# Performance work log

Measured on AMD Instinct MI355X. Metric: run time of the kernel, lower is better.

## Reference

```python
import jax, jax.numpy as jnp
import numpy as np

FIELD = 7  # field_size


def _conv1x1(x, w):
    # x: [b,c,h,w], w: [c_out,c_in] (1x1 conv, no bias)
    return jnp.einsum('bchw,oc->bohw', x, w)


def _patches(x, f):
    # torch unfold with 'same' padding: output [b, c*f*f, h, w], channel-major
    # (feature index = c*f*f + kh*f + kw), matching KAIR extract_image_patches
    # layout for odd f / stride 1 (symmetric pad (f-1)//2).
    return jax.lax.conv_general_dilated_patches(
        x, filter_shape=(f, f), window_strides=(1, 1), padding='SAME',
        dimension_numbers=('NCHW', 'OIHW', 'NCHW'))


def setup_inputs() -> dict:
    key = jax.random.key(0)
    k0, k1, k2, k3, k4 = jax.random.split(key, 5)
    c, ci = 256, 128
    b, h, w = 4, 64, 64
    s = 1.0 / np.sqrt(c)
    si = 1.0 / np.sqrt(ci)
    return {
        'x': jax.random.normal(k0, (b, c, h, w), dtype=jnp.float32),
        'w_phi': jax.random.normal(k1, (ci, c), dtype=jnp.float32) * s,
        'w_theta': jax.random.normal(k2, (ci, c), dtype=jnp.float32) * s,
        'w_g': jax.random.normal(k3, (ci, c), dtype=jnp.float32) * s,
        'w_mask': jax.random.normal(k4, (c, ci), dtype=jnp.float32) * si,
    }


def reference(x, w_phi, w_theta, w_g, w_mask):
    b, c, h, w = x.shape
    ci = w_phi.shape[0]
    f = FIELD
    kk = f * f

    x_phi = _conv1x1(x, w_phi)      # [b,ci,h,w]
    x_g = _conv1x1(x, w_g)          # [b,ci,h,w]
    x_theta = _conv1x1(x, w_theta)  # [b,ci,h,w]

    # theta: unsqueeze(-2) then permute(0,2,4,3,1) -> [b,h,w,1,ci]
    q = jnp.transpose(x_theta, (0, 2, 3, 1))[:, :, :, None, :]

    # phi patches: [b, ci*kk, h, w] reshaped (row-major, faithful to torch
    # reshape of the unfold output) to [b,h,w,ci,kk]
    p_phi = _patches(x_phi, f).reshape(b, h, w, ci, kk)
    scores = jnp.matmul(q, p_phi)                 # [b,h,w,1,kk]
    attn = jax.nn.softmax(scores, axis=1)         # softmax over dim=1 (h), faithful

    p_g = _patches(x_g, f).reshape(b, h, w, kk, ci)
    out = jnp.matmul(attn, p_g)                   # [b,h,w,1,ci]

    # permute(0,4,3,1,2).view(b,ci,h,w)
    y = jnp.transpose(out, (0, 4, 3, 1, 2)).reshape(b, ci, h, w)
    mask = _conv1x1(y, w_mask)                    # [b,c,h,w]
    return mask + x
```

## Files before the change

### kernel.cpp

```cpp
#include <hip/hip_runtime.h>


#define PLANE    5040
#define A_BATCH  645120

typedef __attribute__((ext_vector_type(8))) short short8;
typedef __attribute__((ext_vector_type(4))) float floatx4;

__device__ __forceinline__ float bf2f(unsigned short u) {
    union { unsigned int i; float f; } v; v.i = ((unsigned int)u) << 16; return v.f;
}
__device__ __forceinline__ unsigned short f2bf(float f) {
    union { float f; unsigned int i; } v; v.f = f;
    unsigned int r = v.i + 0x7FFFu + ((v.i >> 16) & 1u);
    return (unsigned short)(r >> 16);
}

__global__ __launch_bounds__(256) void prep_kernel(
    const float* __restrict__ x,
    const float* __restrict__ w_phi,
    const float* __restrict__ w_theta,
    const float* __restrict__ w_g,
    const float* __restrict__ w_mask,
    unsigned short* __restrict__ xp_hi,
    unsigned short* __restrict__ xp_lo,
    unsigned short* __restrict__ w3p_hi,
    unsigned short* __restrict__ w3p_lo,
    unsigned short* __restrict__ wmp_hi,
    unsigned short* __restrict__ wmp_lo,
    uint4* __restrict__ zero_region)
{
    const int tid = threadIdx.x;
    const int bx = blockIdx.x;

    if (bx < 1024) {
        const int b  = bx >> 8;
        const int kt = (bx >> 6) & 3;
        const int pt = bx & 63;
        __shared__ float tile[64][65];
        #pragma unroll
        for (int i = 0; i < 16; ++i) {
            int lin = tid + i * 256;
            int kk = lin >> 6, pp = lin & 63;
            tile[kk][pp] = x[(b * 256 + kt * 64 + kk) * 4096 + pt * 64 + pp];
        }
        __syncthreads();
        #pragma unroll
        for (int i = 0; i < 16; ++i) {
            int lin = tid + i * 256;
            int frag = lin >> 9;
            int idx  = lin & 511;
            int kbL  = frag >> 2;
            int ptL  = frag & 3;
            int j    = idx & 7;
            int n    = (idx >> 3) & 15;
            int quad = idx >> 7;
            float f = tile[kbL * 32 + quad * 8 + j][ptL * 16 + n];
            unsigned short h = f2bf(f);
            int addr = ((b * 8 + kt * 2 + kbL) * 256 + pt * 4 + ptL) * 512 + idx;
            xp_hi[addr] = h;
            xp_lo[addr] = f2bf(f - bf2f(h));
        }
    } else {
        const int wid = (bx - 1024) * 256 + tid;
        for (int e = wid; e < 98304; e += 32768) {
            int frag = e >> 9;
            int idx  = e & 511;
            int nt16 = frag >> 3, kb = frag & 7;
            int j = idx & 7, m = (idx >> 3) & 15, quad = idx >> 7;
            int n = nt16 * 16 + m;
            int k = kb * 32 + quad * 8 + j;
            float v = (n < 128) ? w_phi[n * 256 + k]
                    : (n < 256) ? w_theta[(n - 128) * 256 + k]
                                : w_g[(n - 256) * 256 + k];
            unsigned short h = f2bf(v);
            w3p_hi[e] = h;
            w3p_lo[e] = f2bf(v - bf2f(h));
        }
        {
            int e = wid;
            int frag = e >> 9;
            int idx  = e & 511;
            int ot16 = frag >> 2, kb = frag & 3;
            int j = idx & 7, m = (idx >> 3) & 15, quad = idx >> 7;
            float v = w_mask[(ot16 * 16 + m) * 128 + kb * 32 + quad * 8 + j];
            unsigned short h = f2bf(v);
            wmp_hi[e] = h;
            wmp_lo[e] = f2bf(v - bf2f(h));
        }
        const uint4 z = make_uint4(0u, 0u, 0u, 0u);
        for (int i = wid; i < 645120; i += 32768) zero_region[i] = z;
    }
}

__global__ __launch_bounds__(256) void conv3_mfma_kernel(
    const unsigned short* __restrict__ xp_hi,
    const unsigned short* __restrict__ xp_lo,
    const unsigned short* __restrict__ w3p_hi,
    const unsigned short* __restrict__ w3p_lo,
    unsigned short* __restrict__ A_phi,
    unsigned short* __restrict__ theta_bf,
    unsigned short* __restrict__ A_g)
{
    const int tid = threadIdx.x;
    const int w   = tid >> 6;
    const int ln  = tid & 63;
    const int lm  = ln & 15;
    const int quad = ln >> 4;
    const int bx = blockIdx.x;
    const int nt = blockIdx.y;
    const int b  = blockIdx.z;
    const int nt16a = nt * 8 + w;
    const int nt16b = nt * 8 + 4 + w;
    const int lnofs = ln * 8;

    floatx4 accA[4] = {{0.f,0.f,0.f,0.f},{0.f,0.f,0.f,0.f},
                       {0.f,0.f,0.f,0.f},{0.f,0.f,0.f,0.f}};
    floatx4 accB[4] = {{0.f,0.f,0.f,0.f},{0.f,0.f,0.f,0.f},
                       {0.f,0.f,0.f,0.f},{0.f,0.f,0.f,0.f}};

    #pragma unroll
    for (int kb = 0; kb < 8; ++kb) {
        const int aoffA = (nt16a * 8 + kb) * 512 + lnofs;
        const int aoffB = (nt16b * 8 + kb) * 512 + lnofs;
        const int boff  = ((b * 8 + kb) * 256 + bx * 4) * 512 + lnofs;
        short8 ahA = *reinterpret_cast<const short8*>(w3p_hi + aoffA);
        short8 alA = *reinterpret_cast<const short8*>(w3p_lo + aoffA);
        short8 ahB = *reinterpret_cast<const short8*>(w3p_hi + aoffB);
        short8 alB = *reinterpret_cast<const short8*>(w3p_lo + aoffB);
        short8 bh[4], bl[4];
        #pragma unroll
        for (int ct = 0; ct < 4; ++ct) {
            bh[ct] = *reinterpret_cast<const short8*>(xp_hi + boff + ct * 512);
            bl[ct] = *reinterpret_cast<const short8*>(xp_lo + boff + ct * 512);
        }
        #pragma unroll
        for (int ct = 0; ct < 4; ++ct) {
            accA[ct] = __builtin_amdgcn_mfma_f32_16x16x32_bf16(ahA, bh[ct], accA[ct], 0, 0, 0);
            accA[ct] = __builtin_amdgcn_mfma_f32_16x16x32_bf16(ahA, bl[ct], accA[ct], 0, 0, 0);
            accA[ct] = __builtin_amdgcn_mfma_f32_16x16x32_bf16(alA, bh[ct], accA[ct], 0, 0, 0);
            accB[ct] = __builtin_amdgcn_mfma_f32_16x16x32_bf16(ahB, bh[ct], accB[ct], 0, 0, 0);
            accB[ct] = __builtin_amdgcn_mfma_f32_16x16x32_bf16(ahB, bl[ct], accB[ct], 0, 0, 0);
            accB[ct] = __builtin_amdgcn_mfma_f32_16x16x32_bf16(alB, bh[ct], accB[ct], 0, 0, 0);
        }
    }

    const int py = bx;
    if (nt == 1) {
        #pragma unroll
        for (int ct = 0; ct < 4; ++ct) {
            const int p = bx * 64 + ct * 16 + lm;
            #pragma unroll
            for (int reg = 0; reg < 4; ++reg) {
                const int r = w * 16 + quad * 4 + reg;
                theta_bf[(b * 4096 + p) * 128 + r]      = f2bf(accA[ct][reg]);
                theta_bf[(b * 4096 + p) * 128 + r + 64] = f2bf(accB[ct][reg]);
            }
        }
    } else {
        unsigned short* __restrict__ A = (nt == 0) ? A_phi : A_g;
        #pragma unroll
        for (int ct = 0; ct < 4; ++ct) {
            const int pxx = ct * 16 + lm;
            #pragma unroll
            for (int reg = 0; reg < 4; ++reg) {
                const int r = w * 16 + quad * 4 + reg;
                A[b * A_BATCH + r * PLANE + (py + 3) * 72 + pxx + 4] =
                    f2bf(accA[ct][reg]);
                A[b * A_BATCH + (r + 64) * PLANE + (py + 3) * 72 + pxx + 4] =
                    f2bf(accB[ct][reg]);
            }
        }
    }
}

__global__ __launch_bounds__(256, 8) void scores_kernel(
    const unsigned short* __restrict__ Apad,
    const unsigned short* __restrict__ theta_bf,
    float* __restrict__ scores)
{
    const int w  = threadIdx.x >> 6;
    const int ln = threadIdx.x & 63;
    const int s  = blockIdx.x * 4 + w;
    const int b  = blockIdx.y;

    __shared__ float th[4][128];
    {
        const unsigned short* tb = theta_bf + (b * 4096 + s) * 128;
        th[w][ln]      = bf2f(tb[ln]);
        th[w][ln + 64] = bf2f(tb[ln + 64]);
    }
    __syncthreads();

    const unsigned short* __restrict__ Ab = Apad + b * A_BATCH;

    const int base  = s * 6272;
    const int ch_lo = base >> 12;
    const unsigned B1 = (unsigned)(ch_lo + 1) << 12;
    const unsigned B2 = (unsigned)(ch_lo + 2) << 12;
    const int d1 = (int)B1 - base;
    const int d2 = d1 + 4096;

    int A1 = d1 / 49;
    int A2 = (d1 + 48) / 49;
    int C1 = d2 / 49;        if (C1 > 128) C1 = 128;
    int C2 = (d2 + 48) / 49; if (C2 > 128) C2 = 128;

    unsigned OFFv[3];
    #pragma unroll
    for (int i = 0; i < 3; ++i) {
        int ch = ch_lo + i;
        int c0 = ch / 49; if (c0 > 127) c0 = 127;
        int rr = ch - c0 * 49;
        int kh = rr / 7;
        int kw = rr - kh * 7;
        OFFv[i] = (unsigned)(c0 * PLANE + kh * 72 + kw + 1);
    }

    unsigned F = (unsigned)(base + ln);
    float acc = 0.f;

    {
        const unsigned OFF_ = OFFv[0];
        #pragma unroll 4
        for (int cc = 0; cc < A1; ++cc) {
            unsigned p = F & 4095u;
            unsigned a = OFF_ + p + ((p >> 6) << 3);
            acc = fmaf(th[w][cc], bf2f(Ab[a]), acc);
            F += 49u;
        }
    }
    for (int cc = A1; cc < A2; ++cc) {
        unsigned OFF_ = (F >= B1) ? OFFv[1] : OFFv[0];
        unsigned p = F & 4095u;
        unsigned a = OFF_ + p + ((p >> 6) << 3);
        acc = fmaf(th[w][cc], bf2f(Ab[a]), acc);
        F += 49u;
    }
    {
        const unsigned OFF_ = OFFv[1];
        #pragma unroll 4
        for (int cc = A2; cc < C1; ++cc) {
            unsigned p = F & 4095u;
            unsigned a = OFF_ + p + ((p >> 6) << 3);
            acc = fmaf(th[w][cc], bf2f(Ab[a]), acc);
            F += 49u;
        }
    }
    for (int cc = C1; cc < C2; ++cc) {
        unsigned OFF_ = (F >= B2) ? OFFv[2] : OFFv[1];
        unsigned p = F & 4095u;
        unsigned a = OFF_ + p + ((p >> 6) << 3);
        acc = fmaf(th[w][cc], bf2f(Ab[a]), acc);
        F += 49u;
    }
    {
        const unsigned OFF_ = OFFv[2];
        #pragma unroll 4
        for (int cc = C2; cc < 128; ++cc) {
            unsigned p = F & 4095u;
            unsigned a = OFF_ + p + ((p >> 6) << 3);
            acc = fmaf(th[w][cc], bf2f(Ab[a]), acc);
            F += 49u;
        }
    }

    if (ln < 49) scores[(b * 4096 + s) * 64 + ln] = acc;
}

__global__ __launch_bounds__(256) void softmax_stats_kernel(
    const float* __restrict__ scores,
    float* __restrict__ m_arr,
    float* __restrict__ inv_arr)
{
    const int b = blockIdx.x >> 6;
    const int j = blockIdx.x & 63;
    const int tid = threadIdx.x;
    const int wv = tid >> 6;
    const int ln = tid & 63;

    __shared__ float tile[64][52];

    #pragma unroll
    for (int it = 0; it < 16; ++it) {
        int i = it * 4 + wv;
        if (ln < 49) tile[i][ln] = scores[(b * 4096 + i * 64 + j) * 64 + ln];
    }
    __syncthreads();

    if (tid < 49) {
        float m = -3.4e38f;
        #pragma unroll 8
        for (int i = 0; i < 64; ++i) m = fmaxf(m, tile[i][tid]);
        float sum = 0.f;
        #pragma unroll 8
        for (int i = 0; i < 64; ++i) sum += __expf(tile[i][tid] - m);
        m_arr[(b * 64 + j) * 49 + tid]   = m;
        inv_arr[(b * 64 + j) * 49 + tid] = 1.f / sum;
    }
}

__global__ __launch_bounds__(1024) void agg_mask_kernel(
    const float* __restrict__ scores,
    const float* __restrict__ m_arr,
    const float* __restrict__ inv_arr,
    const unsigned short* __restrict__ Apad,
    const unsigned short* __restrict__ wmp_hi,
    const unsigned short* __restrict__ wmp_lo,
    const float* __restrict__ x,
    float* __restrict__ out)
{
    const int tid = threadIdx.x;
    const int blk = blockIdx.x;
    const int b   = blockIdx.y;
    const int P0  = blk * 32;

    __shared__ float at_l[32][52];
    __shared__ unsigned short y_lds[8 * 512];

    const int j0 = P0 & 63;
    #pragma unroll
    for (int it = 0; it < 2; ++it) {
        int idx = tid + it * 1024;
        int lp = idx >> 6;
        int t  = idx & 63;
        if (t < 49) {
            const int s = P0 + lp;
            const int j = j0 + lp;
            float sc = scores[(b * 4096 + s) * 64 + t];
            float m  = m_arr[(b * 64 + j) * 49 + t];
            float iv = inv_arr[(b * 64 + j) * 49 + t];
            at_l[lp][t] = __expf(sc - m) * iv;
        }
    }
    __syncthreads();

    const unsigned short* __restrict__ Ab = Apad + b * A_BATCH;
    const int pq = tid >> 7;
    const int cc = tid & 127;

    #pragma unroll
    for (int rep = 0; rep < 4; ++rep) {
        const int lp = rep * 8 + pq;
        const int s  = P0 + lp;

        const int base  = s * 6272;
        const int ch_lo = base >> 12;
        const unsigned B1 = (unsigned)(ch_lo + 1) << 12;
        const unsigned B2 = (unsigned)(ch_lo + 2) << 12;
        const int d1 = (int)B1 - base;
        const int d2 = d1 + 4096;

        int A1 = d1 >> 7;
        int A2 = (d1 + 127) >> 7;
        int C1 = d2 >> 7;          if (C1 > 49) C1 = 49;
        int C2 = (d2 + 127) >> 7;  if (C2 > 49) C2 = 49;
        if (A1 > 49) A1 = 49;
        if (A2 > 49) A2 = 49;

        unsigned OFFv[3];
        #pragma unroll
        for (int i = 0; i < 3; ++i) {
            int ch = ch_lo + i;
            int c0 = ch / 49; if (c0 > 127) c0 = 127;
            int rr = ch - c0 * 49;
            int kh = rr / 7;
            int kw = rr - kh * 7;
            OFFv[i] = (unsigned)(c0 * PLANE + kh * 72 + kw + 1);
        }

        float acc = 0.f;

        {
            unsigned p0 = (unsigned)(base + cc) & 4095u;
            unsigned a = OFFv[0] + p0 + ((p0 >> 6) << 3);
            #pragma unroll 4
            for (int t = 0; t < A1; ++t) {
                acc = fmaf(at_l[lp][t], bf2f(Ab[a]), acc);
                a += 144u;
            }
        }
        for (int t = A1; t < A2; ++t) {
            unsigned F = (unsigned)(base + cc) + 128u * (unsigned)t;
            unsigned OFF_ = (F >= B1) ? OFFv[1] : OFFv[0];
            unsigned p = F & 4095u;
            unsigned a = OFF_ + p + ((p >> 6) << 3);
            acc = fmaf(at_l[lp][t], bf2f(Ab[a]), acc);
        }
        {
            unsigned F = (unsigned)(base + cc) + 128u * (unsigned)A2;
            unsigned p0 = F & 4095u;
            unsigned a = OFFv[1] + p0 + ((p0 >> 6) << 3);
            #pragma unroll 4
            for (int t = A2; t < C1; ++t) {
                acc = fmaf(at_l[lp][t], bf2f(Ab[a]), acc);
                a += 144u;
            }
        }
        for (int t = C1; t < C2; ++t) {
            unsigned F = (unsigned)(base + cc) + 128u * (unsigned)t;
            unsigned OFF_ = (F >= B2) ? OFFv[2] : OFFv[1];
            unsigned p = F & 4095u;
            unsigned a = OFF_ + p + ((p >> 6) << 3);
            acc = fmaf(at_l[lp][t], bf2f(Ab[a]), acc);
        }
        {
            unsigned F = (unsigned)(base + cc) + 128u * (unsigned)C2;
            unsigned p0 = F & 4095u;
            unsigned a = OFFv[2] + p0 + ((p0 >> 6) << 3);
            #pragma unroll 4
            for (int t = C2; t < 49; ++t) {
                acc = fmaf(at_l[lp][t], bf2f(Ab[a]), acc);
                a += 144u;
            }
        }

        const int kb = cc >> 5, k32 = cc & 31;
        const int quad = k32 >> 3, jx = k32 & 7;
        const int ct = lp >> 4, n = lp & 15;
        y_lds[(kb * 2 + ct) * 512 + (quad * 16 + n) * 8 + jx] = f2bf(acc);
    }
    __syncthreads();

    const int w    = tid >> 6;
    const int ln   = tid & 63;
    const int lm   = ln & 15;
    const int quad = ln >> 4;
    const int lnofs = ln * 8;

    floatx4 accA[2] = {{0.f,0.f,0.f,0.f},{0.f,0.f,0.f,0.f}};

    #pragma unroll
    for (int kb = 0; kb < 4; ++kb) {
        const int aoffA = (w * 4 + kb) * 512 + lnofs;
        short8 ahA = *reinterpret_cast<const short8*>(wmp_hi + aoffA);
        short8 alA = *reinterpret_cast<const short8*>(wmp_lo + aoffA);
        short8 bf[2];
        #pragma unroll
        for (int ct = 0; ct < 2; ++ct)
            bf[ct] = *reinterpret_cast<const short8*>(
                y_lds + (kb * 2 + ct) * 512 + lnofs);
        #pragma unroll
        for (int ct = 0; ct < 2; ++ct) {
            accA[ct] = __builtin_amdgcn_mfma_f32_16x16x32_bf16(ahA, bf[ct], accA[ct], 0, 0, 0);
            accA[ct] = __builtin_amdgcn_mfma_f32_16x16x32_bf16(alA, bf[ct], accA[ct], 0, 0, 0);
        }
    }

    #pragma unroll
    for (int ct = 0; ct < 2; ++ct) {
        const int p = P0 + ct * 16 + lm;
        #pragma unroll
        for (int reg = 0; reg < 4; ++reg) {
            const int oA = w * 16 + quad * 4 + reg;
            const int ofsA = (b * 256 + oA) * 4096 + p;
            out[ofsA] = accA[ct][reg] + x[ofsA];
        }
    }
}

extern "C" void kernel_launch(void* const* d_in, const int* in_sizes, int n_in,
                              void* d_out, int out_size, void* d_ws, size_t ws_size,
                              hipStream_t stream) {
    const float* x       = (const float*)d_in[0];
    const float* w_phi   = (const float*)d_in[1];
    const float* w_theta = (const float*)d_in[2];
    const float* w_g     = (const float*)d_in[3];
    const float* w_mask  = (const float*)d_in[4];

    float* out_f = (float*)d_out;

    unsigned short* ws_u  = (unsigned short*)d_ws;
    unsigned short* A_phi = ws_u;
    unsigned short* A_g   = ws_u + 2580480;
    unsigned short* th_u  = ws_u + 7258112;
    float*          sc_f  = (float*)(ws_u + 9355264);
    unsigned short* xph   = ws_u + 11452416;
    unsigned short* xpl   = ws_u + 15646720;
    unsigned short* w3ph  = ws_u + 19841024;
    unsigned short* w3pl  = ws_u + 19939328;
    unsigned short* wmph  = ws_u + 20037632;
    unsigned short* wmpl  = ws_u + 20070400;
    float*          m_f   = (float*)(ws_u + 20103168);
    float*          inv_f = (float*)(ws_u + 20128256);

    hipLaunchKernelGGL(prep_kernel, dim3(1152), dim3(256), 0, stream,
                       x, w_phi, w_theta, w_g, w_mask,
                       xph, xpl, w3ph, w3pl, wmph, wmpl, (uint4*)A_phi);
    hipLaunchKernelGGL(conv3_mfma_kernel, dim3(64, 3, 4), dim3(256), 0, stream,
                       xph, xpl, w3ph, w3pl, A_phi, th_u, A_g);
    hipLaunchKernelGGL(scores_kernel, dim3(1024, 4), dim3(256), 0, stream,
                       A_phi, th_u, sc_f);
    hipLaunchKernelGGL(softmax_stats_kernel, dim3(256), dim3(256), 0, stream,
                       sc_f, m_f, inv_f);
    hipLaunchKernelGGL(agg_mask_kernel, dim3(128, 4), dim3(1024), 0, stream,
                       sc_f, m_f, inv_f, A_g, wmph, wmpl, x, out_f);
}
```

Baseline: 162.5 us.

## Stage phi patch window in shared memory for scores kernel with 16 pixels per block

```diff
diff --git a/kernel.cpp b/kernel.cpp
--- a/kernel.cpp
+++ b/kernel.cpp
@@ -14,6 +14,14 @@
     union { float f; unsigned int i; } v; v.f = f;
     unsigned int r = v.i + 0x7FFFu + ((v.i >> 16) & 1u);
     return (unsigned short)(r >> 16);
+}
+
+__device__ __forceinline__ unsigned off_of_ch(int ch) {
+    int c0 = ch / 49; if (c0 > 127) c0 = 127;
+    int rr = ch - c0 * 49;
+    int kh = rr / 7;
+    int kw = rr - kh * 7;
+    return (unsigned)(c0 * PLANE + kh * 72 + kw + 1);
 }
 
 __global__ __launch_bounds__(256) void prep_kernel(
@@ -174,25 +182,40 @@
     }
 }
 
-__global__ __launch_bounds__(256, 8) void scores_kernel(
+__global__ __launch_bounds__(1024, 8) void scores_kernel(
     const unsigned short* __restrict__ Apad,
     const unsigned short* __restrict__ theta_bf,
     float* __restrict__ scores)
 {
-    const int w  = threadIdx.x >> 6;
-    const int ln = threadIdx.x & 63;
-    const int s  = blockIdx.x * 4 + w;
-    const int b  = blockIdx.y;
-
-    __shared__ float th[4][128];
+    const int tid = threadIdx.x;
+    const int w   = tid >> 6;
+    const int ln  = tid & 63;
+    const int s0  = blockIdx.x * 16;
+    const int b   = blockIdx.y;
+    const int s   = s0 + w;
+
+    __shared__ float th[16][128];
+    __shared__ unsigned short sA[9600];
+
     {
-        const unsigned short* tb = theta_bf + (b * 4096 + s) * 128;
-        th[w][ln]      = bf2f(tb[ln]);
-        th[w][ln + 64] = bf2f(tb[ln + 64]);
+        int idx = tid * 2;
+        int lp = idx >> 7, cc = idx & 127;
+        const unsigned short* tb = theta_bf + (b * 4096 + s0 + lp) * 128 + cc;
+        th[lp][cc]     = bf2f(tb[0]);
+        th[lp][cc + 1] = bf2f(tb[1]);
+    }
+
+    const int chB_lo = (s0 * 6272) >> 12;
+    int chB_hi = ((s0 + 15) * 6272 + 6286) >> 12;
+    if (chB_hi > 6271) chB_hi = 6271;
+    const unsigned a_base = off_of_ch(chB_lo);
+    const int cnt = (int)(off_of_ch(chB_hi) + 4599u - a_base) + 1;
+
+    {
+        const unsigned short* src = Apad + b * A_BATCH + a_base;
+        for (int i = tid; i < cnt; i += 1024) sA[i] = src[i];
     }
     __syncthreads();
-
-    const unsigned short* __restrict__ Ab = Apad + b * A_BATCH;
 
     const int base  = s * 6272;
     const int ch_lo = base >> 12;
@@ -208,14 +231,8 @@
 
     unsigned OFFv[3];
     #pragma unroll
-    for (int i = 0; i < 3; ++i) {
-        int ch = ch_lo + i;
-        int c0 = ch / 49; if (c0 > 127) c0 = 127;
-        int rr = ch - c0 * 49;
-        int kh = rr / 7;
-        int kw = rr - kh * 7;
-        OFFv[i] = (unsigned)(c0 * PLANE + kh * 72 + kw + 1);
-    }
+    for (int i = 0; i < 3; ++i)
+        OFFv[i] = off_of_ch(ch_lo + i) - a_base;
 
     unsigned F = (unsigned)(base + ln);
     float acc = 0.f;
@@ -226,7 +243,7 @@
         for (int cc = 0; cc < A1; ++cc) {
             unsigned p = F & 4095u;
             unsigned a = OFF_ + p + ((p >> 6) << 3);
-            acc = fmaf(th[w][cc], bf2f(Ab[a]), acc);
+            acc = fmaf(th[w][cc], bf2f(sA[a]), acc);
             F += 49u;
         }
     }
@@ -234,7 +251,7 @@
         unsigned OFF_ = (F >= B1) ? OFFv[1] : OFFv[0];
         unsigned p = F & 4095u;
         unsigned a = OFF_ + p + ((p >> 6) << 3);
-        acc = fmaf(th[w][cc], bf2f(Ab[a]), acc);
+        acc = fmaf(th[w][cc], bf2f(sA[a]), acc);
         F += 49u;
     }
     {
@@ -243,7 +260,7 @@
         for (int cc = A2; cc < C1; ++cc) {
             unsigned p = F & 4095u;
             unsigned a = OFF_ + p + ((p >> 6) << 3);
-            acc = fmaf(th[w][cc], bf2f(Ab[a]), acc);
+            acc = fmaf(th[w][cc], bf2f(sA[a]), acc);
             F += 49u;
         }
     }
@@ -251,7 +268,7 @@
         unsigned OFF_ = (F >= B2) ? OFFv[2] : OFFv[1];
         unsigned p = F & 4095u;
         unsigned a = OFF_ + p + ((p >> 6) << 3);
-        acc = fmaf(th[w][cc], bf2f(Ab[a]), acc);
+        acc = fmaf(th[w][cc], bf2f(sA[a]), acc);
         F += 49u;
     }
     {
@@ -260,7 +277,7 @@
         for (int cc = C2; cc < 128; ++cc) {
             unsigned p = F & 4095u;
             unsigned a = OFF_ + p + ((p >> 6) << 3);
-            acc = fmaf(th[w][cc], bf2f(Ab[a]), acc);
+            acc = fmaf(th[w][cc], bf2f(sA[a]), acc);
             F += 49u;
         }
     }
@@ -489,7 +506,7 @@
                        xph, xpl, w3ph, w3pl, wmph, wmpl, (uint4*)A_phi);
     hipLaunchKernelGGL(conv3_mfma_kernel, dim3(64, 3, 4), dim3(256), 0, stream,
                        xph, xpl, w3ph, w3pl, A_phi, th_u, A_g);
-    hipLaunchKernelGGL(scores_kernel, dim3(1024, 4), dim3(256), 0, stream,
+    hipLaunchKernelGGL(scores_kernel, dim3(256, 4), dim3(1024), 0, stream,
                        A_phi, th_u, sc_f);
     hipLaunchKernelGGL(softmax_stats_kernel, dim3(256), dim3(256), 0, stream,
                        sc_f, m_f, inv_f);
```

After: 159.1 us. 2.0% less time.
